# Kernel optimization log

Measured on AMD Instinct MI355X. Metric: run time of the kernel, lower is better.

The kernel has to match this reference:

```python
import jax, jax.numpy as jnp
import numpy as np

EPS = 1e-10


def setup_inputs() -> dict:
    key = jax.random.key(0)
    k1, k2 = jax.random.split(key)
    x = jax.random.normal(k1, (8, 16, 512, 512), dtype=jnp.float32)
    # inv_grid in [-1, 1], grid_sample-style normalized coordinates
    inv_grid = jax.random.uniform(k2, (8, 512, 512, 2), dtype=jnp.float32,
                                  minval=-1.0, maxval=1.0)
    return {"x": x, "inv_grid": inv_grid}


def reference(x, inv_grid):
    bs, nc, h, w = x.shape  # OH=OW=None -> output spatial dims = input dims
    g = (inv_grid + 1.0) * 0.5
    # map to padded pixel coords and clamp, exactly as the torch module
    gi = jnp.clip(g[..., 0] * h + 1.0, 0.0, h + 1 - 2 * EPS).reshape(-1)
    gj = jnp.clip(g[..., 1] * w + 1.0, 0.0, w + 1 - 2 * EPS).reshape(-1)
    ii = gi.astype(jnp.int32)  # floor (coords are non-negative)
    jj = gj.astype(jnp.int32)
    npix = inv_grid.shape[1] * inv_grid.shape[2]
    b_idx = jnp.repeat(jnp.arange(bs, dtype=jnp.int32), npix)
    H3, W3 = h + 3, w + 3
    Bflat = jnp.zeros((bs * H3 * W3,), dtype=jnp.float32)
    # 4-corner bilinear splat scatter-add; denominator is channel-independent
    for di in (0, 1):
        wi = jax.nn.relu(1.0 - jnp.abs(gi - (ii + di).astype(gi.dtype)))
        for dj in (0, 1):
            wj = jax.nn.relu(1.0 - jnp.abs(gj - (jj + dj).astype(gj.dtype)))
            idx = (b_idx * H3 + (ii + di)) * W3 + (jj + dj)
            Bflat = Bflat.at[idx].add(wi * wj)
    Bden = Bflat.reshape(bs, H3, W3)[:, 1:h + 1, 1:w + 1]
    # torch adds the same B_ch to every channel -> broadcast over C
    return jnp.broadcast_to(Bden[:, None], (bs, nc, h, w))
```

## Files before the change

### kernel.cpp

```cpp
#include <hip/hip_runtime.h>

#define BS 8
#define NC 16
#define H 512
#define W 512
#define RB 17
#define TPB 31
#define NKH 62
#define CHUNKS 1024
#define CHPB 128
#define CPTS 2048
#define CAP 3072
#define ACC_ROWS 19
#define ACC_W 264
#define ACC_ELEMS (ACC_ROWS * ACC_W)
#define GRID2 (BS * TPB)
#define FIX_SCALE 16777216.0f
#define FIX_INV   5.9604644775390625e-8f
#define INV512    0.001953125f

typedef float f32x4 __attribute__((ext_vector_type(4)));


__global__ __launch_bounds__(512)
void k1_bin(const float* __restrict__ inv_grid,
            unsigned* __restrict__ bins,
            unsigned* __restrict__ chunkOff) {
    __shared__ __align__(16) unsigned stage[CAP];
    __shared__ unsigned cnt[NKH];
    __shared__ unsigned off[64];
    const int blk = blockIdx.x, tid = threadIdx.x;
    if (tid < NKH) cnt[tid] = 0;
    __syncthreads();

    const float4* src = reinterpret_cast<const float4*>(inv_grid)
                      + (size_t)blk * (CPTS / 2);
    unsigned rec0[4];
    unsigned dk[4][4];
#pragma unroll
    for (int i = 0; i < 2; ++i) {
        float4 v = src[tid + i * 512];
#pragma unroll
        for (int s = 0; s < 2; ++s) {
            const int p = i * 2 + s;
            float gx = s ? v.z : v.x;
            float gy = s ? v.w : v.y;
            float gi = fminf(fmaxf((gx + 1.0f) * 0.5f * (float)H + 1.0f, 0.0f), 513.0f);
            float gj = fminf(fmaxf((gy + 1.0f) * 0.5f * (float)W + 1.0f, 0.0f), 513.0f);
            int ii = (int)gi, jj = (int)gj;
            int k = ii / RB;
            bool rd = (ii - k * RB == RB - 1);
            int h = (jj >= 256) ? 1 : 0;
            bool cd = (jj == 256);
            unsigned fi9 = (unsigned)((gi - (float)ii) * 512.0f + 0.5f);
            if (fi9 > 511u) fi9 = 511u;
            unsigned fj9 = (unsigned)((gj - (float)jj) * 512.0f + 0.5f);
            if (fj9 > 511u) fj9 = 511u;
            unsigned il = (unsigned)(ii - k * RB + 1);
            unsigned jl = (unsigned)(jj - (h << 8));
            rec0[p] = (il << 27) | (fi9 << 18) | (jl << 9) | fj9;
            unsigned bk0 = (unsigned)(2 * k + h);
            dk[p][0] = (bk0 << 13) | atomicAdd(&cnt[bk0], 1u);
            dk[p][1] = dk[p][2] = dk[p][3] = 0xFFFFFFFFu;
            if (rd) dk[p][1] = ((bk0 + 2) << 13) | atomicAdd(&cnt[bk0 + 2], 1u);
            if (cd) { dk[p][2] = ((bk0 - 1) << 13) | atomicAdd(&cnt[bk0 - 1], 1u);
                if (rd) dk[p][3] = ((bk0 + 1) << 13) | atomicAdd(&cnt[bk0 + 1], 1u); }
        }
    }
    __syncthreads();
    if (tid < 64) {
        unsigned v = (tid < NKH) ? cnt[tid] : 0u;
#pragma unroll
        for (int d = 1; d < 64; d <<= 1) {
            unsigned o = __shfl_up(v, d, 64);
            if (tid >= d) v += o;
        }
        if (tid == 0) off[0] = 0u;
        if (tid < 63) off[tid + 1] = v;
    }
    __syncthreads();
    if (tid < 63) chunkOff[blk * 64 + tid] = off[tid];
    const unsigned ADJ1 = 0u - (17u << 27);
    const unsigned ADJ2 = (256u << 9);
    const unsigned adj[4] = {0u, ADJ1, ADJ2, ADJ1 + ADJ2};
#pragma unroll
    for (int p = 0; p < 4; ++p)
#pragma unroll
        for (int q = 0; q < 4; ++q) {
            unsigned d = dk[p][q];
            if (d != 0xFFFFFFFFu) {
                unsigned pos = off[d >> 13] + (d & 8191u);
                if (pos < CAP) stage[pos] = rec0[p] + adj[q];
            }
        }
    __syncthreads();
    unsigned total = off[62];
    if (total > CAP) total = CAP;
    const unsigned nvec = (total + 3u) >> 2;
    uint4* dst4 = reinterpret_cast<uint4*>(bins + (size_t)blk * CAP);
    const uint4* st4 = reinterpret_cast<const uint4*>(stage);
    for (unsigned i = tid; i < nvec; i += 512) dst4[i] = st4[i];
}

__device__ __forceinline__ void splat_half(const unsigned* __restrict__ bins,
                                           unsigned* acc,
                                           const unsigned* segs, const unsigned* segn,
                                           int bBase, int tid) {
    const int g = tid >> 4, lane = tid & 15;
#pragma unroll
    for (int pass = 0; pass < 2; ++pass) {
        const int seg = g + pass * 64;
        const unsigned* base = bins + (size_t)(bBase + seg) * CAP + segs[seg];
        const unsigned n = segn[seg];
        for (unsigned idx = lane; idx < n; idx += 16) {
            unsigned rec = base[idx];
            unsigned il = rec >> 27;
            float fi = (float)((rec >> 18) & 511u) * INV512;
            unsigned jl = (rec >> 9) & 511u;
            float fj = (float)(rec & 511u) * INV512;
            float a = 1.0f - fi, c = 1.0f - fj;
            unsigned ofs = il * ACC_W + jl + 3;
            atomicAdd(&acc[ofs],             (unsigned)(a  * c  * FIX_SCALE + 0.5f));
            atomicAdd(&acc[ofs + 1],         (unsigned)(a  * fj * FIX_SCALE + 0.5f));
            atomicAdd(&acc[ofs + ACC_W],     (unsigned)(fi * c  * FIX_SCALE + 0.5f));
            atomicAdd(&acc[ofs + ACC_W + 1], (unsigned)(fi * fj * FIX_SCALE + 0.5f));
        }
    }
}

__device__ __forceinline__ void store_half(const unsigned* acc, float* __restrict__ out,
                                           int b, int r0, int h, int tid) {
    const int l = tid & 63, wv = tid >> 6;
    for (int it = wv; it < RB * NC; it += 16) {
        int d = it >> 4, c = it & 15;
        int r = r0 + d;
        if (r < 1 || r > H) continue;
        const unsigned* ap = acc + (d + 1) * ACC_W + 4 + 4 * l;
        uint4 q = *reinterpret_cast<const uint4*>(ap);
        f32x4 v;
        v.x = (float)q.x * FIX_INV; v.y = (float)q.y * FIX_INV;
        v.z = (float)q.z * FIX_INV; v.w = (float)q.w * FIX_INV;
        size_t o = (((size_t)(b * NC + c)) * H + (r - 1)) * (size_t)W
                 + (h << 8) + 4 * l;
        *reinterpret_cast<f32x4*>(out + o) = v;
    }
}

__global__ __launch_bounds__(1024)
void k2_splat_store(const unsigned* __restrict__ bins,
                    const unsigned* __restrict__ chunkOff,
                    float* __restrict__ out) {
    __shared__ unsigned accA[ACC_ELEMS], accB[ACC_ELEMS];
    __shared__ unsigned sA[CHPB], nA[CHPB], sB[CHPB], nB[CHPB];
    const int blk = blockIdx.x;
    const int b = blk / TPB, k = blk % TPB;
    const int r0 = k * RB;
    const int tid = threadIdx.x;

    for (int i = tid; i < ACC_ELEMS; i += 1024) { accA[i] = 0u; accB[i] = 0u; }
    if (tid < CHPB) {
        const unsigned* row = chunkOff + (size_t)(b * CHPB + tid) * 64;
        unsigned x0 = row[2 * k], x1 = row[2 * k + 1], x2 = row[2 * k + 2];
        sA[tid] = x0; nA[tid] = x1 - x0;
        sB[tid] = x1; nB[tid] = x2 - x1;
    }
    __syncthreads();

    splat_half(bins, accA, sA, nA, b * CHPB, tid);
    __syncthreads();
    store_half(accA, out, b, r0, 0, tid);
    splat_half(bins, accB, sB, nB, b * CHPB, tid);
    __syncthreads();
    store_half(accB, out, b, r0, 1, tid);
}

extern "C" void kernel_launch(void* const* d_in, const int* in_sizes, int n_in,
                              void* d_out, int out_size, void* d_ws, size_t ws_size,
                              hipStream_t stream) {
    const float* inv_grid = (const float*)d_in[1];
    float* out = (float*)d_out;

    unsigned* bins     = (unsigned*)d_ws;
    unsigned* chunkOff = (unsigned*)((char*)d_ws + (size_t)CHUNKS * CAP * sizeof(unsigned));

    k1_bin<<<CHUNKS, 512, 0, stream>>>(inv_grid, bins, chunkOff);
    k2_splat_store<<<GRID2, 1024, 0, stream>>>(bins, chunkOff, out);
}
```

Before: 40.34 us.

## Shrink splat tiles to 8 rows and split halves into separate blocks

Row-band height drops from 17 to 8 and each column half becomes its own 256-thread block, so the splat grid grows from 248 to 1040 blocks. Bin indexing uses shifts, and the bin-offset prefix scan is widened to three wavefronts to cover 130 bins. The aim is better occupancy and less serial work per block in the splat/store kernel. In exchange, more points fall on band boundaries and get duplicated, each block reads a smaller slice from all 128 chunks, and only 2 threads walk each chunk segment.

```diff
diff --git a/kernel.cpp b/kernel.cpp
--- a/kernel.cpp
+++ b/kernel.cpp
@@ -4,17 +4,18 @@
 #define NC 16
 #define H 512
 #define W 512
-#define RB 17
-#define TPB 31
-#define NKH 62
+#define RB 8
+#define NKB 65
+#define NBK 130
+#define COFF 132
 #define CHUNKS 1024
 #define CHPB 128
 #define CPTS 2048
 #define CAP 3072
-#define ACC_ROWS 19
+#define ACC_ROWS 10
 #define ACC_W 264
 #define ACC_ELEMS (ACC_ROWS * ACC_W)
-#define GRID2 (BS * TPB)
+#define GRID2 (BS * NBK)
 #define FIX_SCALE 16777216.0f
 #define FIX_INV   5.9604644775390625e-8f
 #define INV512    0.001953125f
@@ -27,10 +28,11 @@
             unsigned* __restrict__ bins,
             unsigned* __restrict__ chunkOff) {
     __shared__ __align__(16) unsigned stage[CAP];
-    __shared__ unsigned cnt[NKH];
-    __shared__ unsigned off[64];
+    __shared__ unsigned cnt[NBK];
+    __shared__ unsigned incl[192];
+    __shared__ unsigned off[NBK + 1];
     const int blk = blockIdx.x, tid = threadIdx.x;
-    if (tid < NKH) cnt[tid] = 0;
+    if (tid < NBK) cnt[tid] = 0;
     __syncthreads();
 
     const float4* src = reinterpret_cast<const float4*>(inv_grid)
@@ -48,39 +50,51 @@
             float gi = fminf(fmaxf((gx + 1.0f) * 0.5f * (float)H + 1.0f, 0.0f), 513.0f);
             float gj = fminf(fmaxf((gy + 1.0f) * 0.5f * (float)W + 1.0f, 0.0f), 513.0f);
             int ii = (int)gi, jj = (int)gj;
-            int k = ii / RB;
-            bool rd = (ii - k * RB == RB - 1);
+            int k = ii >> 3;
+            bool rd = (ii & 7) == 7;
             int h = (jj >= 256) ? 1 : 0;
             bool cd = (jj == 256);
             unsigned fi9 = (unsigned)((gi - (float)ii) * 512.0f + 0.5f);
             if (fi9 > 511u) fi9 = 511u;
             unsigned fj9 = (unsigned)((gj - (float)jj) * 512.0f + 0.5f);
             if (fj9 > 511u) fj9 = 511u;
-            unsigned il = (unsigned)(ii - k * RB + 1);
+            unsigned il = (unsigned)(ii - (k << 3) + 1);
             unsigned jl = (unsigned)(jj - (h << 8));
             rec0[p] = (il << 27) | (fi9 << 18) | (jl << 9) | fj9;
             unsigned bk0 = (unsigned)(2 * k + h);
-            dk[p][0] = (bk0 << 13) | atomicAdd(&cnt[bk0], 1u);
+            dk[p][0] = (bk0 << 12) | atomicAdd(&cnt[bk0], 1u);
             dk[p][1] = dk[p][2] = dk[p][3] = 0xFFFFFFFFu;
-            if (rd) dk[p][1] = ((bk0 + 2) << 13) | atomicAdd(&cnt[bk0 + 2], 1u);
-            if (cd) { dk[p][2] = ((bk0 - 1) << 13) | atomicAdd(&cnt[bk0 - 1], 1u);
-                if (rd) dk[p][3] = ((bk0 + 1) << 13) | atomicAdd(&cnt[bk0 + 1], 1u); }
+            if (rd) dk[p][1] = ((bk0 + 2) << 12) | atomicAdd(&cnt[bk0 + 2], 1u);
+            if (cd) { dk[p][2] = ((bk0 - 1) << 12) | atomicAdd(&cnt[bk0 - 1], 1u);
+                if (rd) dk[p][3] = ((bk0 + 1) << 12) | atomicAdd(&cnt[bk0 + 1], 1u); }
         }
     }
     __syncthreads();
-    if (tid < 64) {
-        unsigned v = (tid < NKH) ? cnt[tid] : 0u;
+    if (tid < 192) {
+        const int lane = tid & 63, seg = tid >> 6;
+        const int idx = seg * 64 + lane;
+        unsigned v = (idx < NBK) ? cnt[idx] : 0u;
 #pragma unroll
         for (int d = 1; d < 64; d <<= 1) {
             unsigned o = __shfl_up(v, d, 64);
-            if (tid >= d) v += o;
+            if (lane >= d) v += o;
         }
-        if (tid == 0) off[0] = 0u;
-        if (tid < 63) off[tid + 1] = v;
+        incl[tid] = v;
     }
     __syncthreads();
-    if (tid < 63) chunkOff[blk * 64 + tid] = off[tid];
-    const unsigned ADJ1 = 0u - (17u << 27);
+    if (tid <= NBK) {
+        unsigned v = 0u;
+        if (tid > 0) {
+            int j = tid - 1;
+            v = incl[j];
+            if (j >= 64)  v += incl[63];
+            if (j >= 128) v += incl[127];
+        }
+        off[tid] = v;
+        chunkOff[(size_t)blk * COFF + tid] = v;
+    }
+    __syncthreads();
+    const unsigned ADJ1 = 0u - (8u << 27);
     const unsigned ADJ2 = (256u << 9);
     const unsigned adj[4] = {0u, ADJ1, ADJ2, ADJ1 + ADJ2};
 #pragma unroll
@@ -89,12 +103,12 @@
         for (int q = 0; q < 4; ++q) {
             unsigned d = dk[p][q];
             if (d != 0xFFFFFFFFu) {
-                unsigned pos = off[d >> 13] + (d & 8191u);
+                unsigned pos = off[d >> 12] + (d & 4095u);
                 if (pos < CAP) stage[pos] = rec0[p] + adj[q];
             }
         }
     __syncthreads();
-    unsigned total = off[62];
+    unsigned total = off[NBK];
     if (total > CAP) total = CAP;
     const unsigned nvec = (total + 3u) >> 2;
     uint4* dst4 = reinterpret_cast<uint4*>(bins + (size_t)blk * CAP);
@@ -102,37 +116,50 @@
     for (unsigned i = tid; i < nvec; i += 512) dst4[i] = st4[i];
 }
 
-__device__ __forceinline__ void splat_half(const unsigned* __restrict__ bins,
-                                           unsigned* acc,
-                                           const unsigned* segs, const unsigned* segn,
-                                           int bBase, int tid) {
-    const int g = tid >> 4, lane = tid & 15;
-#pragma unroll
-    for (int pass = 0; pass < 2; ++pass) {
-        const int seg = g + pass * 64;
-        const unsigned* base = bins + (size_t)(bBase + seg) * CAP + segs[seg];
-        const unsigned n = segn[seg];
-        for (unsigned idx = lane; idx < n; idx += 16) {
-            unsigned rec = base[idx];
-            unsigned il = rec >> 27;
-            float fi = (float)((rec >> 18) & 511u) * INV512;
-            unsigned jl = (rec >> 9) & 511u;
-            float fj = (float)(rec & 511u) * INV512;
-            float a = 1.0f - fi, c = 1.0f - fj;
-            unsigned ofs = il * ACC_W + jl + 3;
-            atomicAdd(&acc[ofs],             (unsigned)(a  * c  * FIX_SCALE + 0.5f));
-            atomicAdd(&acc[ofs + 1],         (unsigned)(a  * fj * FIX_SCALE + 0.5f));
-            atomicAdd(&acc[ofs + ACC_W],     (unsigned)(fi * c  * FIX_SCALE + 0.5f));
-            atomicAdd(&acc[ofs + ACC_W + 1], (unsigned)(fi * fj * FIX_SCALE + 0.5f));
-        }
+__global__ __launch_bounds__(256)
+void k2_splat_store(const unsigned* __restrict__ bins,
+                    const unsigned* __restrict__ chunkOff,
+                    float* __restrict__ out) {
+    __shared__ unsigned acc[ACC_ELEMS];
+    __shared__ unsigned segs[CHPB], segn[CHPB];
+    const int blk = blockIdx.x;
+    const int b = blk / NBK;
+    const int bk = blk % NBK;
+    const int k = bk >> 1, h = bk & 1;
+    const int r0 = k << 3;
+    const int tid = threadIdx.x;
+
+    for (int i = tid; i < ACC_ELEMS; i += 256) acc[i] = 0u;
+    if (tid < CHPB) {
+        const unsigned* row = chunkOff + (size_t)(b * CHPB + tid) * COFF;
+        unsigned s0 = row[bk];
+        segs[tid] = s0;
+        segn[tid] = row[bk + 1] - s0;
     }
-}
+    __syncthreads();
 
-__device__ __forceinline__ void store_half(const unsigned* acc, float* __restrict__ out,
-                                           int b, int r0, int h, int tid) {
+    const int g = tid >> 1, lane = tid & 1;
+    const unsigned* base = bins + (size_t)(b * CHPB + g) * CAP + segs[g];
+    const unsigned n = segn[g];
+    for (unsigned idx = lane; idx < n; idx += 2) {
+        unsigned rec = base[idx];
+        unsigned il = rec >> 27;
+        float fi = (float)((rec >> 18) & 511u) * INV512;
+        unsigned jl = (rec >> 9) & 511u;
+        float fj = (float)(rec & 511u) * INV512;
+        float a = 1.0f - fi, c = 1.0f - fj;
+        unsigned ofs = il * ACC_W + jl + 3;
+        atomicAdd(&acc[ofs],             (unsigned)(a  * c  * FIX_SCALE + 0.5f));
+        atomicAdd(&acc[ofs + 1],         (unsigned)(a  * fj * FIX_SCALE + 0.5f));
+        atomicAdd(&acc[ofs + ACC_W],     (unsigned)(fi * c  * FIX_SCALE + 0.5f));
+        atomicAdd(&acc[ofs + ACC_W + 1], (unsigned)(fi * fj * FIX_SCALE + 0.5f));
+    }
+    __syncthreads();
+
     const int l = tid & 63, wv = tid >> 6;
-    for (int it = wv; it < RB * NC; it += 16) {
-        int d = it >> 4, c = it & 15;
+    for (int it = 0; it < 32; ++it) {
+        int c = (wv << 2) + (it >> 3);
+        int d = it & 7;
         int r = r0 + d;
         if (r < 1 || r > H) continue;
         const unsigned* ap = acc + (d + 1) * ACC_W + 4 + 4 * l;
@@ -146,34 +173,6 @@
     }
 }
 
-__global__ __launch_bounds__(1024)
-void k2_splat_store(const unsigned* __restrict__ bins,
-                    const unsigned* __restrict__ chunkOff,
-                    float* __restrict__ out) {
-    __shared__ unsigned accA[ACC_ELEMS], accB[ACC_ELEMS];
-    __shared__ unsigned sA[CHPB], nA[CHPB], sB[CHPB], nB[CHPB];
-    const int blk = blockIdx.x;
-    const int b = blk / TPB, k = blk % TPB;
-    const int r0 = k * RB;
-    const int tid = threadIdx.x;
-
-    for (int i = tid; i < ACC_ELEMS; i += 1024) { accA[i] = 0u; accB[i] = 0u; }
-    if (tid < CHPB) {
-        const unsigned* row = chunkOff + (size_t)(b * CHPB + tid) * 64;
-        unsigned x0 = row[2 * k], x1 = row[2 * k + 1], x2 = row[2 * k + 2];
-        sA[tid] = x0; nA[tid] = x1 - x0;
-        sB[tid] = x1; nB[tid] = x2 - x1;
-    }
-    __syncthreads();
-
-    splat_half(bins, accA, sA, nA, b * CHPB, tid);
-    __syncthreads();
-    store_half(accA, out, b, r0, 0, tid);
-    splat_half(bins, accB, sB, nB, b * CHPB, tid);
-    __syncthreads();
-    store_half(accB, out, b, r0, 1, tid);
-}
-
 extern "C" void kernel_launch(void* const* d_in, const int* in_sizes, int n_in,
                               void* d_out, int out_size, void* d_ws, size_t ws_size,
                               hipStream_t stream) {
@@ -184,5 +183,5 @@
     unsigned* chunkOff = (unsigned*)((char*)d_ws + (size_t)CHUNKS * CAP * sizeof(unsigned));
 
     k1_bin<<<CHUNKS, 512, 0, stream>>>(inv_grid, bins, chunkOff);
-    k2_splat_store<<<GRID2, 1024, 0, stream>>>(bins, chunkOff, out);
+    k2_splat_store<<<GRID2, 256, 0, stream>>>(bins, chunkOff, out);
 }
```

Result: slower. 46.45 us (+15.2%).
